# Kernel tuning notes

Hardware: AMD Instinct MI355X
Metric: run time of the kernel (lower is better)

The kernel has to match this reference:

```python
import jax, jax.numpy as jnp
import numpy as np

B, N, D = 4, 2048, 4
COUPLING = 1.0
DT = 1.0


def setup_inputs() -> dict:
    key = jax.random.key(0)
    k1, k2, k3, k4 = jax.random.split(key, 4)
    theta_prev = jax.random.normal(k1, (B, N, D), dtype=jnp.float32)
    gamma_t = jax.random.normal(k2, (B, N, D), dtype=jnp.float32)
    affinity = jax.random.uniform(k3, (B, N, N), dtype=jnp.float32)
    alpha_t = jax.random.normal(k4, (B, N, N), dtype=jnp.float32)
    # learned parameters, initialized as in the torch module
    omega = jnp.zeros((N, D), dtype=jnp.float32)
    kappa = jnp.ones((N, D), dtype=jnp.float32)
    alpha_bias = jnp.zeros((N, N), dtype=jnp.float32)
    return {
        "theta_prev": theta_prev,
        "gamma_t": gamma_t,
        "affinity": affinity,
        "alpha_t": alpha_t,
        "omega": omega,
        "kappa": kappa,
        "alpha_bias": alpha_bias,
    }


def reference(theta_prev, gamma_t, affinity, alpha_t, omega, kappa, alpha_bias):
    # theta_prev: [B, N, D], affinity/alpha_t: [B, N, N]
    n = theta_prev.shape[1]
    alpha_total = alpha_t + alpha_bias[None, :, :]               # [B, N, N]
    # phase_term[b, i, j, d] = sin(theta[b, j, d] - theta[b, i, d] - alpha_total[b, i, j])
    phase_term = jnp.sin(
        theta_prev[:, None, :, :] - theta_prev[:, :, None, :]
        - alpha_total[:, :, :, None]
    )                                                            # [B, N, N, D]
    coupling_term = (COUPLING / n) * jnp.einsum(
        "bij,bijd->bid", affinity, phase_term
    )                                                            # [B, N, D]
    drive_term = kappa[None, :, :] * (gamma_t - theta_prev)
    theta_dot = omega[None, :, :] + drive_term + coupling_term
    return theta_prev + DT * theta_dot
```

## Files before the change

### kernel.cpp

```cpp
#include <hip/hip_runtime.h>

#define BB 4
#define NN 2048
#define DD 4
#define QQ (NN / 4)
#define BLOCK 256
#define JIT (QQ / 64)

typedef float f4 __attribute__((ext_vector_type(4)));
typedef _Float16 h8 __attribute__((ext_vector_type(8)));

__global__ __launch_bounds__(BLOCK) void precomp(const float* __restrict__ theta,
                                                 float* __restrict__ sArr,
                                                 float* __restrict__ cArr,
                                                 h8* __restrict__ scT) {
    const int t = blockIdx.x * BLOCK + threadIdx.x;
    const int b = t / QQ, q = t % QQ;
    const f4* theta4 = (const f4*)theta;
    f4* s4 = (f4*)sArr;
    f4* c4 = (f4*)cArr;

    float s[4][4], c[4][4];
    #pragma unroll
    for (int u = 0; u < 4; ++u) {
        const f4 th = theta4[(size_t)b * NN + 4 * q + u];
        const float thA[4] = {th.x, th.y, th.z, th.w};
        #pragma unroll
        for (int d = 0; d < 4; ++d) __sincosf(thA[d], &s[u][d], &c[u][d]);
    }
    #pragma unroll
    for (int u = 0; u < 4; ++u) {
        f4 sv, cv;
        sv.x = s[u][0]; sv.y = s[u][1]; sv.z = s[u][2]; sv.w = s[u][3];
        cv.x = c[u][0]; cv.y = c[u][1]; cv.z = c[u][2]; cv.w = c[u][3];
        s4[(size_t)b * NN + 4 * q + u] = sv;
        c4[(size_t)b * NN + 4 * q + u] = cv;
    }
    #pragma unroll
    for (int d = 0; d < 4; ++d) {
        h8 w;
        #pragma unroll
        for (int u = 0; u < 4; ++u) {
            w[2 * u]     = (_Float16)s[u][d];
            w[2 * u + 1] = (_Float16)c[u][d];
        }
        scT[((size_t)b * 4 + d) * QQ + q] = w;
    }
}

__global__ __launch_bounds__(BLOCK) void kuramoto_main(
    const float* __restrict__ theta,
    const float* __restrict__ gam,
    const float* __restrict__ aff,
    const float* __restrict__ alp,
    const float* __restrict__ omega,
    const float* __restrict__ kappa,
    const float* __restrict__ bias,
    const float* __restrict__ sArr,
    const float* __restrict__ cArr,
    const h8* __restrict__ scT,
    float* __restrict__ out)
{
    const int x   = blockIdx.x;
    const int low = x & 31;
    const int b   = low >> 3;
    const int g   = (x >> 5) * 8 + (low & 7);
    const int i0  = g * 8;

    const int tid  = threadIdx.x;
    const int wave = tid >> 6;
    const int lane = tid & 63;
    const int r0   = i0 + 2 * wave;

    const f4* aff4 = (const f4*)(aff + (size_t)b * NN * NN);
    const f4* alp4 = (const f4*)(alp + (size_t)b * NN * NN);
    const f4* bia4 = (const f4*)bias;
    const h8* scb  = scT + (size_t)b * 4 * QQ;

    float accU[2][4], accV[2][4];
    #pragma unroll
    for (int r = 0; r < 2; ++r)
        #pragma unroll
        for (int d = 0; d < 4; ++d) { accU[r][d] = 0.f; accV[r][d] = 0.f; }

    f4 av[2][2], lv[2][2], bv[2][2];
    {
        const int q = lane;
        #pragma unroll
        for (int r = 0; r < 2; ++r) {
            const size_t qo = (size_t)(r0 + r) * QQ + q;
            av[0][r] = __builtin_nontemporal_load(&aff4[qo]);
            lv[0][r] = __builtin_nontemporal_load(&alp4[qo]);
            bv[0][r] = bia4[qo];
        }
    }

    #pragma unroll
    for (int jj = 0; jj < JIT; ++jj) {
        const int cur = jj & 1;
        const int nxt = cur ^ 1;
        const int q   = lane + 64 * jj;

        if (jj + 1 < JIT) {
            const int qn = lane + 64 * (jj + 1);
            #pragma unroll
            for (int r = 0; r < 2; ++r) {
                const size_t qo = (size_t)(r0 + r) * QQ + qn;
                av[nxt][r] = __builtin_nontemporal_load(&aff4[qo]);
                lv[nxt][r] = __builtin_nontemporal_load(&alp4[qo]);
                bv[nxt][r] = bia4[qo];
            }
        }

        float sj[4][4], cj[4][4];
        #pragma unroll
        for (int d = 0; d < 4; ++d) {
            const h8 w = scb[(size_t)d * QQ + q];
            #pragma unroll
            for (int u = 0; u < 4; ++u) {
                sj[u][d] = (float)w[2 * u];
                cj[u][d] = (float)w[2 * u + 1];
            }
        }

        #pragma unroll
        for (int r = 0; r < 2; ++r) {
            const f4 alr = lv[cur][r] + bv[cur][r];
            const float aA[4] = {av[cur][r].x, av[cur][r].y, av[cur][r].z, av[cur][r].w};
            const float lA[4] = {alr.x, alr.y, alr.z, alr.w};
            #pragma unroll
            for (int u = 0; u < 4; ++u) {
                float sa, ca;
                __sincosf(lA[u], &sa, &ca);
                const float wc = aA[u] * ca;
                const float ws = aA[u] * sa;
                #pragma unroll
                for (int d = 0; d < 4; ++d) {
                    accU[r][d] = fmaf(wc, sj[u][d], fmaf(-ws, cj[u][d], accU[r][d]));
                    accV[r][d] = fmaf(wc, cj[u][d], fmaf(ws, sj[u][d], accV[r][d]));
                }
            }
        }
    }

    #pragma unroll
    for (int r = 0; r < 2; ++r)
        #pragma unroll
        for (int d = 0; d < 4; ++d) {
            float u = accU[r][d], v = accV[r][d];
            #pragma unroll
            for (int off = 32; off >= 1; off >>= 1) {
                u += __shfl_down(u, off, 64);
                v += __shfl_down(v, off, 64);
            }
            accU[r][d] = u; accV[r][d] = v;
        }

    if (lane == 0) {
        const f4* theta4 = (const f4*)theta;
        const f4* gam4   = (const f4*)gam;
        const f4* om4    = (const f4*)omega;
        const f4* kp4    = (const f4*)kappa;
        const f4* s4     = (const f4*)sArr;
        const f4* c4     = (const f4*)cArr;
        f4* out4         = (f4*)out;
        #pragma unroll
        for (int r = 0; r < 2; ++r) {
            const int i = r0 + r;
            const size_t base = (size_t)b * NN + i;
            const f4 th = theta4[base];
            const f4 gm = gam4[base];
            const f4 om = om4[i];
            const f4 kp = kp4[i];
            const f4 si = s4[base];
            const f4 ci = c4[base];
            const float siA[4] = {si.x, si.y, si.z, si.w};
            const float ciA[4] = {ci.x, ci.y, ci.z, ci.w};
            const float thA[4] = {th.x, th.y, th.z, th.w};
            const float gmA[4] = {gm.x, gm.y, gm.z, gm.w};
            const float omA[4] = {om.x, om.y, om.z, om.w};
            const float kpA[4] = {kp.x, kp.y, kp.z, kp.w};
            f4 o;
            float oA[4];
            #pragma unroll
            for (int d = 0; d < 4; ++d) {
                const float coup = (1.0f / (float)NN) * (ciA[d] * accU[r][d] - siA[d] * accV[r][d]);
                oA[d] = thA[d] + omA[d] + kpA[d] * (gmA[d] - thA[d]) + coup;
            }
            o.x = oA[0]; o.y = oA[1]; o.z = oA[2]; o.w = oA[3];
            out4[base] = o;
        }
    }
}

extern "C" void kernel_launch(void* const* d_in, const int* in_sizes, int n_in,
                              void* d_out, int out_size, void* d_ws, size_t ws_size,
                              hipStream_t stream) {
    const float* theta = (const float*)d_in[0];
    const float* gam   = (const float*)d_in[1];
    const float* aff   = (const float*)d_in[2];
    const float* alp   = (const float*)d_in[3];
    const float* omega = (const float*)d_in[4];
    const float* kappa = (const float*)d_in[5];
    const float* bias  = (const float*)d_in[6];
    float* out  = (float*)d_out;

    float* sArr = (float*)d_ws;
    float* cArr = sArr + BB * NN * DD;
    h8*    scT  = (h8*)(cArr + BB * NN * DD);

    precomp<<<(BB * QQ) / BLOCK, BLOCK, 0, stream>>>(theta, sArr, cArr, scT);
    kuramoto_main<<<BB * (NN / 8), BLOCK, 0, stream>>>(
        theta, gam, aff, alp, omega, kappa, bias, sArr, cArr, scT, out);
}
```

Before: 173.2 us.

## Stage per-batch sin/cos table in LDS and assign one row per wave

The main kernel now copies the batch's packed fp16 sin/cos table (32 KB) into shared memory once per block and reads it from LDS in the inner loop instead of global memory. Each wave now handles one output row instead of two, the grid doubles, and launch bounds ask for 5 blocks per CU. The goal is to raise occupancy and memory-level parallelism for the streaming affinity/alpha reads. The cost is a per-block table copy and sync, and 32 KB of LDS per block limits how many blocks fit on a CU.

```diff
diff --git a/kernel.cpp b/kernel.cpp
--- a/kernel.cpp
+++ b/kernel.cpp
@@ -24,15 +24,14 @@
     #pragma unroll
     for (int u = 0; u < 4; ++u) {
         const f4 th = theta4[(size_t)b * NN + 4 * q + u];
-        const float thA[4] = {th.x, th.y, th.z, th.w};
         #pragma unroll
-        for (int d = 0; d < 4; ++d) __sincosf(thA[d], &s[u][d], &c[u][d]);
+        for (int d = 0; d < 4; ++d) __sincosf(th[d], &s[u][d], &c[u][d]);
     }
     #pragma unroll
     for (int u = 0; u < 4; ++u) {
         f4 sv, cv;
-        sv.x = s[u][0]; sv.y = s[u][1]; sv.z = s[u][2]; sv.w = s[u][3];
-        cv.x = c[u][0]; cv.y = c[u][1]; cv.z = c[u][2]; cv.w = c[u][3];
+        #pragma unroll
+        for (int d = 0; d < 4; ++d) { sv[d] = s[u][d]; cv[d] = c[u][d]; }
         s4[(size_t)b * NN + 4 * q + u] = sv;
         c4[(size_t)b * NN + 4 * q + u] = cv;
     }
@@ -48,7 +47,7 @@
     }
 }
 
-__global__ __launch_bounds__(BLOCK) void kuramoto_main(
+__global__ __launch_bounds__(BLOCK, 5) void kuramoto_main(
     const float* __restrict__ theta,
     const float* __restrict__ gam,
     const float* __restrict__ aff,
@@ -65,35 +64,33 @@
     const int low = x & 31;
     const int b   = low >> 3;
     const int g   = (x >> 5) * 8 + (low & 7);
-    const int i0  = g * 8;
+    const int i0  = g * 4;
 
     const int tid  = threadIdx.x;
     const int wave = tid >> 6;
     const int lane = tid & 63;
-    const int r0   = i0 + 2 * wave;
+    const int i    = i0 + wave;
 
-    const f4* aff4 = (const f4*)(aff + (size_t)b * NN * NN);
-    const f4* alp4 = (const f4*)(alp + (size_t)b * NN * NN);
-    const f4* bia4 = (const f4*)bias;
-    const h8* scb  = scT + (size_t)b * 4 * QQ;
+    __shared__ h8 lsc[4 * QQ];
+    {
+        const h8* gsc = scT + (size_t)b * 4 * QQ;
+        #pragma unroll
+        for (int k = 0; k < (4 * QQ) / BLOCK; ++k)
+            lsc[tid + BLOCK * k] = gsc[tid + BLOCK * k];
+    }
+    __syncthreads();
 
-    float accU[2][4], accV[2][4];
-    #pragma unroll
-    for (int r = 0; r < 2; ++r)
-        #pragma unroll
-        for (int d = 0; d < 4; ++d) { accU[r][d] = 0.f; accV[r][d] = 0.f; }
+    const f4* arow = (const f4*)(aff + (size_t)b * NN * NN) + (size_t)i * QQ;
+    const f4* lrow = (const f4*)(alp + (size_t)b * NN * NN) + (size_t)i * QQ;
+    const f4* brow = (const f4*)bias + (size_t)i * QQ;
 
-    f4 av[2][2], lv[2][2], bv[2][2];
-    {
-        const int q = lane;
-        #pragma unroll
-        for (int r = 0; r < 2; ++r) {
-            const size_t qo = (size_t)(r0 + r) * QQ + q;
-            av[0][r] = __builtin_nontemporal_load(&aff4[qo]);
-            lv[0][r] = __builtin_nontemporal_load(&alp4[qo]);
-            bv[0][r] = bia4[qo];
-        }
-    }
+    f4 accU = {0.f, 0.f, 0.f, 0.f};
+    f4 accV = {0.f, 0.f, 0.f, 0.f};
+
+    f4 av[2], lv[2], bv[2];
+    av[0] = __builtin_nontemporal_load(&arow[lane]);
+    lv[0] = __builtin_nontemporal_load(&lrow[lane]);
+    bv[0] = brow[lane];
 
     #pragma unroll
     for (int jj = 0; jj < JIT; ++jj) {
@@ -102,20 +99,16 @@
         const int q   = lane + 64 * jj;
 
         if (jj + 1 < JIT) {
-            const int qn = lane + 64 * (jj + 1);
-            #pragma unroll
-            for (int r = 0; r < 2; ++r) {
-                const size_t qo = (size_t)(r0 + r) * QQ + qn;
-                av[nxt][r] = __builtin_nontemporal_load(&aff4[qo]);
-                lv[nxt][r] = __builtin_nontemporal_load(&alp4[qo]);
-                bv[nxt][r] = bia4[qo];
-            }
+            const int qn = q + 64;
+            av[nxt] = __builtin_nontemporal_load(&arow[qn]);
+            lv[nxt] = __builtin_nontemporal_load(&lrow[qn]);
+            bv[nxt] = brow[qn];
         }
 
-        float sj[4][4], cj[4][4];
+        f4 sj[4], cj[4];
         #pragma unroll
         for (int d = 0; d < 4; ++d) {
-            const h8 w = scb[(size_t)d * QQ + q];
+            const h8 w = lsc[d * QQ + q];
             #pragma unroll
             for (int u = 0; u < 4; ++u) {
                 sj[u][d] = (float)w[2 * u];
@@ -123,38 +116,27 @@
             }
         }
 
+        const f4 alr = lv[cur] + bv[cur];
+        const f4 af  = av[cur];
         #pragma unroll
-        for (int r = 0; r < 2; ++r) {
-            const f4 alr = lv[cur][r] + bv[cur][r];
-            const float aA[4] = {av[cur][r].x, av[cur][r].y, av[cur][r].z, av[cur][r].w};
-            const float lA[4] = {alr.x, alr.y, alr.z, alr.w};
-            #pragma unroll
-            for (int u = 0; u < 4; ++u) {
-                float sa, ca;
-                __sincosf(lA[u], &sa, &ca);
-                const float wc = aA[u] * ca;
-                const float ws = aA[u] * sa;
-                #pragma unroll
-                for (int d = 0; d < 4; ++d) {
-                    accU[r][d] = fmaf(wc, sj[u][d], fmaf(-ws, cj[u][d], accU[r][d]));
-                    accV[r][d] = fmaf(wc, cj[u][d], fmaf(ws, sj[u][d], accV[r][d]));
-                }
-            }
+        for (int u = 0; u < 4; ++u) {
+            float sa, ca;
+            __sincosf(alr[u], &sa, &ca);
+            const float wc = af[u] * ca;
+            const float ws = af[u] * sa;
+            accU += wc * sj[u] - ws * cj[u];
+            accV += wc * cj[u] + ws * sj[u];
         }
     }
 
     #pragma unroll
-    for (int r = 0; r < 2; ++r)
+    for (int off = 32; off >= 1; off >>= 1) {
         #pragma unroll
         for (int d = 0; d < 4; ++d) {
-            float u = accU[r][d], v = accV[r][d];
-            #pragma unroll
-            for (int off = 32; off >= 1; off >>= 1) {
-                u += __shfl_down(u, off, 64);
-                v += __shfl_down(v, off, 64);
-            }
-            accU[r][d] = u; accV[r][d] = v;
+            accU[d] += __shfl_down(accU[d], off, 64);
+            accV[d] += __shfl_down(accV[d], off, 64);
         }
+    }
 
     if (lane == 0) {
         const f4* theta4 = (const f4*)theta;
@@ -164,32 +146,21 @@
         const f4* s4     = (const f4*)sArr;
         const f4* c4     = (const f4*)cArr;
         f4* out4         = (f4*)out;
+
+        const size_t base = (size_t)b * NN + i;
+        const f4 th = theta4[base];
+        const f4 gm = gam4[base];
+        const f4 om = om4[i];
+        const f4 kp = kp4[i];
+        const f4 si = s4[base];
+        const f4 ci = c4[base];
+        f4 o;
         #pragma unroll
-        for (int r = 0; r < 2; ++r) {
-            const int i = r0 + r;
-            const size_t base = (size_t)b * NN + i;
-            const f4 th = theta4[base];
-            const f4 gm = gam4[base];
-            const f4 om = om4[i];
-            const f4 kp = kp4[i];
-            const f4 si = s4[base];
-            const f4 ci = c4[base];
-            const float siA[4] = {si.x, si.y, si.z, si.w};
-            const float ciA[4] = {ci.x, ci.y, ci.z, ci.w};
-            const float thA[4] = {th.x, th.y, th.z, th.w};
-            const float gmA[4] = {gm.x, gm.y, gm.z, gm.w};
-            const float omA[4] = {om.x, om.y, om.z, om.w};
-            const float kpA[4] = {kp.x, kp.y, kp.z, kp.w};
-            f4 o;
-            float oA[4];
-            #pragma unroll
-            for (int d = 0; d < 4; ++d) {
-                const float coup = (1.0f / (float)NN) * (ciA[d] * accU[r][d] - siA[d] * accV[r][d]);
-                oA[d] = thA[d] + omA[d] + kpA[d] * (gmA[d] - thA[d]) + coup;
-            }
-            o.x = oA[0]; o.y = oA[1]; o.z = oA[2]; o.w = oA[3];
-            out4[base] = o;
+        for (int d = 0; d < 4; ++d) {
+            const float coup = (1.0f / (float)NN) * (ci[d] * accU[d] - si[d] * accV[d]);
+            o[d] = th[d] + om[d] + kp[d] * (gm[d] - th[d]) + coup;
         }
+        out4[base] = o;
     }
 }
 
@@ -210,6 +181,6 @@
     h8*    scT  = (h8*)(cArr + BB * NN * DD);
 
     precomp<<<(BB * QQ) / BLOCK, BLOCK, 0, stream>>>(theta, sArr, cArr, scT);
-    kuramoto_main<<<BB * (NN / 8), BLOCK, 0, stream>>>(
+    kuramoto_main<<<BB * (NN / 4), BLOCK, 0, stream>>>(
         theta, gam, aff, alp, omega, kappa, bias, sArr, cArr, scT, out);
 }
```

New measurement: 169.6 us. 2.1% less time.
